# Kernel optimization log

Hardware: AMD Instinct MI355X
Metric: run time of the kernel (lower is better)

The kernel has to match this reference:

```python
import jax, jax.numpy as jnp
import numpy as np

B, S, D = 64, 1452, 1024
G, K, R = 288, 4, 32
VIS = 1152  # number of vision patch tokens; tail is S - VIS = 300 text tokens
MAX_TOKENS = 300


def setup_inputs() -> dict:
    key = jax.random.key(0)
    k1, k2, k3, k4 = jax.random.split(key, 4)
    hidden_states = jax.random.normal(k1, (B, S, D), dtype=jnp.float32)
    attention_mask = jnp.ones((B, S), dtype=jnp.int32)
    # all batches share the same vision patch range [0, VIS-1]
    patch_range_list = jnp.tile(jnp.array([[0, VIS - 1]], dtype=jnp.int32), (B, 1))
    base = jnp.broadcast_to(jnp.arange(VIS, dtype=jnp.int32).reshape(1, G, K), (B, G, K))
    drop = jax.random.uniform(k2, (B, G, K)) < 0.1
    patch_indices_list_list = jnp.where(drop, jnp.int32(-1), base)
    rem = jax.random.randint(k3, (B, R), 0, VIS, dtype=jnp.int32)
    rem = jnp.where(jax.random.uniform(k4, (B, R)) < 0.25, jnp.int32(-1), rem)
    return {
        "hidden_states": hidden_states,
        "attention_mask": attention_mask,
        "patch_range_list": patch_range_list,
        "patch_indices_list_list": patch_indices_list_list,
        "remove_index_list_list": rem,
    }


def reference(hidden_states, attention_mask, patch_range_list, patch_indices_list_list, remove_index_list_list):
    Bn, Sn, Dn = hidden_states.shape
    _, Gn, Kn = patch_indices_list_list.shape
    # vision_end_token_index is taken from batch 0 in the original and used for a
    # shape-defining slice; treat as static (identical across batches here).
    vis_end = int(patch_range_list[0, 1]) + 1

    start = patch_range_list[:, 0]            # [B]
    end = patch_range_list[:, 1]              # [B]
    L = end - start + 1                       # [B] length of sliced hidden_state

    idx = patch_indices_list_list             # [B,G,K]
    mask = idx != -1                          # [B,G,K]
    # remove_index_list: drop -1 padding (map to -2 sentinel so it never matches)
    rem = jnp.where(remove_index_list_list == -1, jnp.int32(-2), remove_index_list_list)  # [B,R]
    in_rem = (idx[..., None] == rem[:, None, None, :]).any(-1)  # torch.isin, [B,G,K]
    mask = mask & ~in_rem

    # torch gather with -1 wraps to the last element of the SLICED hidden_state;
    # replicate exactly (note: the original sums wrapped/removed entries too).
    idx_w = jnp.where(idx >= 0, idx, idx + L[:, None, None])
    gidx = start[:, None, None] + idx_w       # absolute indices into hidden_states
    gathered = jnp.take_along_axis(
        hidden_states, gidx.reshape(Bn, Gn * Kn, 1), axis=1
    ).reshape(Bn, Gn, Kn, Dn)

    cnt = mask.sum(-1)                        # [B,G] divisor = count of kept entries
    pooled = gathered.sum(2) / jnp.maximum(cnt, 1)[..., None].astype(hidden_states.dtype)

    # rows with no valid entries are dropped; survivors are written right-aligned
    valid = mask.any(-1)                      # [B,G]
    n_valid = valid.sum(1)                    # [B]
    rank = jnp.cumsum(valid, axis=1) - 1      # 0-based rank among valid rows
    pos = jnp.where(valid, MAX_TOKENS - n_valid[:, None] + rank, MAX_TOKENS)  # OOB -> drop
    bidx = jnp.arange(Bn)[:, None]

    out_head = jnp.zeros((Bn, MAX_TOKENS, Dn), hidden_states.dtype).at[bidx, pos].set(pooled, mode="drop")
    att_head = jnp.zeros((Bn, MAX_TOKENS), attention_mask.dtype).at[bidx, pos].set(1, mode="drop")

    outputs = jnp.concatenate([out_head, hidden_states[:, vis_end:]], axis=1)
    outputs_attention = jnp.concatenate([att_head, attention_mask[:, vis_end:]], axis=1)
    return outputs, outputs_attention
```

## Files before the change

### kernel.cpp

```cpp
#include <hip/hip_runtime.h>
#include <hip/hip_bf16.h>

#define Bn 64
#define Sn 1452
#define Dn 1024
#define Gn 288
#define Kn 4
#define Rn 32
#define MAXT 300

typedef float f32x4 __attribute__((ext_vector_type(4)));

__global__ void __launch_bounds__(256)
fused2_kernel(const float* __restrict__ hs,
              const int* __restrict__ idx,
              const int* __restrict__ pr,
              const int* __restrict__ rem,
              const int* __restrict__ attn,
              float* __restrict__ out,
              float* __restrict__ att_out,
              int vis_end, int T, int nheadblk, int tail4, int tailrows) {
    const int x = blockIdx.x;
    const int b = blockIdx.y;
    const int tid = threadIdx.x;

    if (x >= nheadblk) {
        const int c = x - nheadblk;
        if (tid < 4) {
            int tr = c * 4 + tid;
            if (tr < tailrows)
                att_out[(size_t)b * T + MAXT + tr] = (float)attn[b * Sn + vis_end + tr];
        }
        const f32x4* src = (const f32x4*)(hs + ((size_t)b * Sn + vis_end) * Dn);
        f32x4* dst = (f32x4*)(out + ((size_t)b * T + MAXT) * Dn);
        const int base = c * 1024;
        f32x4 v0, v1, v2, v3;
        int e0 = base + 0 * 256 + tid;
        int e1 = base + 1 * 256 + tid;
        int e2 = base + 2 * 256 + tid;
        int e3 = base + 3 * 256 + tid;
        bool p0 = e0 < tail4, p1 = e1 < tail4, p2 = e2 < tail4, p3 = e3 < tail4;
        if (p0) v0 = __builtin_nontemporal_load(&src[e0]);
        if (p1) v1 = __builtin_nontemporal_load(&src[e1]);
        if (p2) v2 = __builtin_nontemporal_load(&src[e2]);
        if (p3) v3 = __builtin_nontemporal_load(&src[e3]);
        if (p0) __builtin_nontemporal_store(v0, &dst[e0]);
        if (p1) __builtin_nontemporal_store(v1, &dst[e1]);
        if (p2) __builtin_nontemporal_store(v2, &dst[e2]);
        if (p3) __builtin_nontemporal_store(v3, &dst[e3]);
        return;
    }

    __shared__ int s_rem[Rn];
    __shared__ unsigned long long s_mask[5];
    __shared__ int s_wsum[5];
    __shared__ short s_gor[Gn];
    __shared__ char s_cnt[Gn];

    const int lane = tid & 63;
    const int w = tid >> 6;

    if (tid < Rn) {
        int r = rem[b * Rn + tid];
        s_rem[tid] = (r == -1) ? -2 : r;
    }
    __syncthreads();

    int cnt1 = 0;
    {
        const int g = tid;
#pragma unroll
        for (int k = 0; k < Kn; ++k) {
            int v = idx[(b * Gn + g) * Kn + k];
            bool m = (v != -1);
#pragma unroll
            for (int r = 0; r < Rn; ++r) m = m && (v != s_rem[r]);
            cnt1 += m ? 1 : 0;
        }
        s_cnt[g] = (char)cnt1;
    }
    int cnt2 = 0;
    if (tid < Gn - 256) {
        const int g = 256 + tid;
#pragma unroll
        for (int k = 0; k < Kn; ++k) {
            int v = idx[(b * Gn + g) * Kn + k];
            bool m = (v != -1);
#pragma unroll
            for (int r = 0; r < Rn; ++r) m = m && (v != s_rem[r]);
            cnt2 += m ? 1 : 0;
        }
        s_cnt[g] = (char)cnt2;
    }

    unsigned long long m1 = __ballot(cnt1 > 0);
    if (lane == 0) { s_mask[w] = m1; s_wsum[w] = __popcll(m1); }
    if (w == 0) {
        unsigned long long m2 = __ballot(tid < Gn - 256 && cnt2 > 0);
        if (lane == 0) { s_mask[4] = m2; s_wsum[4] = __popcll(m2); }
    }
    __syncthreads();

    int pre[5], acc = 0;
#pragma unroll
    for (int i = 0; i < 5; ++i) { pre[i] = acc; acc += s_wsum[i]; }
    const int nvalid = acc;
    const int zcut = MAXT - nvalid;

    if (cnt1 > 0) {
        int rank = pre[w] + __popcll(s_mask[w] & ((1ull << lane) - 1ull));
        s_gor[rank] = (short)tid;
    }
    if (tid < Gn - 256 && cnt2 > 0) {
        int rank = pre[4] + __popcll(s_mask[4] & ((1ull << lane) - 1ull));
        s_gor[rank] = (short)(256 + tid);
    }
    __syncthreads();

    if (tid < 2) {
        int t = 2 * x + tid;
        att_out[(size_t)b * T + t] = (t >= zcut) ? 1.0f : 0.0f;
    }

    const int start = pr[b * 2];
    const int L = pr[b * 2 + 1] - start + 1;

#pragma unroll
    for (int i = 0; i < 2; ++i) {
        const int t = 2 * x + i;
        f32x4* outp = (f32x4*)(out + ((size_t)b * T + t) * Dn);
        if (t < zcut) {
            f32x4 z = {0.f, 0.f, 0.f, 0.f};
            __builtin_nontemporal_store(z, &outp[tid]);
            continue;
        }
        const int g = s_gor[t - zcut];
        f32x4 a = {0.f, 0.f, 0.f, 0.f};
#pragma unroll
        for (int k = 0; k < Kn; ++k) {
            int v = idx[(b * Gn + g) * Kn + k];
            int wi = (v >= 0) ? v : v + L;
            const f32x4* row = (const f32x4*)(hs + ((size_t)b * Sn + start + wi) * Dn);
            a += row[tid];
        }
        const int c = (int)s_cnt[g];
        const float scale = 1.0f / (float)((c > 1) ? c : 1);
        a *= scale;
        __builtin_nontemporal_store(a, &outp[tid]);
    }
}

extern "C" void kernel_launch(void* const* d_in, const int* in_sizes, int n_in,
                              void* d_out, int out_size, void* d_ws, size_t ws_size,
                              hipStream_t stream) {
    const float* hs  = (const float*)d_in[0];
    const int* attn  = (const int*)d_in[1];
    const int* pr    = (const int*)d_in[2];
    const int* idx   = (const int*)d_in[3];
    const int* rem   = (const int*)d_in[4];

    float* out = (float*)d_out;

    const int T = out_size / (Bn * (Dn + 1));
    const int vis_end = Sn - (T - MAXT);

    float* att_out = out + (size_t)Bn * T * Dn;

    const int tailrows = T - MAXT;
    const int tail4 = tailrows * (Dn / 4);
    const int ntail = (tailrows + 3) / 4;
    const int nheadblk = (MAXT + 1) / 2;

    fused2_kernel<<<dim3(nheadblk + ntail, Bn), 256, 0, stream>>>(
        hs, idx, pr, rem, attn, out, att_out, vis_end, T, nheadblk, tail4, tailrows);
}
```

Measured before the change: 79.54 us.

## Use shared bitmap for removal lookup and double work per block

Result: slower. 103.6 us (+30.2%).

```diff
diff --git a/kernel.cpp b/kernel.cpp
--- a/kernel.cpp
+++ b/kernel.cpp
@@ -8,11 +8,12 @@
 #define Kn 4
 #define Rn 32
 #define MAXT 300
+#define BMW 18
 
 typedef float f32x4 __attribute__((ext_vector_type(4)));
 
 __global__ void __launch_bounds__(256)
-fused2_kernel(const float* __restrict__ hs,
+fused3_kernel(const float* __restrict__ hs,
               const int* __restrict__ idx,
               const int* __restrict__ pr,
               const int* __restrict__ rem,
@@ -26,32 +27,30 @@
 
     if (x >= nheadblk) {
         const int c = x - nheadblk;
-        if (tid < 4) {
-            int tr = c * 4 + tid;
+        if (tid < 8) {
+            int tr = c * 8 + tid;
             if (tr < tailrows)
                 att_out[(size_t)b * T + MAXT + tr] = (float)attn[b * Sn + vis_end + tr];
         }
         const f32x4* src = (const f32x4*)(hs + ((size_t)b * Sn + vis_end) * Dn);
         f32x4* dst = (f32x4*)(out + ((size_t)b * T + MAXT) * Dn);
-        const int base = c * 1024;
-        f32x4 v0, v1, v2, v3;
-        int e0 = base + 0 * 256 + tid;
-        int e1 = base + 1 * 256 + tid;
-        int e2 = base + 2 * 256 + tid;
-        int e3 = base + 3 * 256 + tid;
-        bool p0 = e0 < tail4, p1 = e1 < tail4, p2 = e2 < tail4, p3 = e3 < tail4;
-        if (p0) v0 = __builtin_nontemporal_load(&src[e0]);
-        if (p1) v1 = __builtin_nontemporal_load(&src[e1]);
-        if (p2) v2 = __builtin_nontemporal_load(&src[e2]);
-        if (p3) v3 = __builtin_nontemporal_load(&src[e3]);
-        if (p0) __builtin_nontemporal_store(v0, &dst[e0]);
-        if (p1) __builtin_nontemporal_store(v1, &dst[e1]);
-        if (p2) __builtin_nontemporal_store(v2, &dst[e2]);
-        if (p3) __builtin_nontemporal_store(v3, &dst[e3]);
+        const int base = c * 2048;
+        f32x4 v[8];
+        int  e[8];
+        bool p[8];
+#pragma unroll
+        for (int j = 0; j < 8; ++j) {
+            e[j] = base + j * 256 + tid;
+            p[j] = e[j] < tail4;
+            if (p[j]) v[j] = __builtin_nontemporal_load(&src[e[j]]);
+        }
+#pragma unroll
+        for (int j = 0; j < 8; ++j)
+            if (p[j]) __builtin_nontemporal_store(v[j], &dst[e[j]]);
         return;
     }
 
-    __shared__ int s_rem[Rn];
+    __shared__ unsigned long long s_bm[BMW];
     __shared__ unsigned long long s_mask[5];
     __shared__ int s_wsum[5];
     __shared__ short s_gor[Gn];
@@ -60,37 +59,42 @@
     const int lane = tid & 63;
     const int w = tid >> 6;
 
+    if (tid < BMW) s_bm[tid] = 0ull;
+    __syncthreads();
     if (tid < Rn) {
         int r = rem[b * Rn + tid];
-        s_rem[tid] = (r == -1) ? -2 : r;
+        if (r >= 0)
+            atomicOr(&s_bm[r >> 6], 1ull << (r & 63));
     }
     __syncthreads();
 
     int cnt1 = 0;
     {
-        const int g = tid;
+        const int4 gi = ((const int4*)idx)[b * Gn + tid];
+        const int vv[4] = {gi.x, gi.y, gi.z, gi.w};
 #pragma unroll
         for (int k = 0; k < Kn; ++k) {
-            int v = idx[(b * Gn + g) * Kn + k];
-            bool m = (v != -1);
-#pragma unroll
-            for (int r = 0; r < Rn; ++r) m = m && (v != s_rem[r]);
-            cnt1 += m ? 1 : 0;
+            int v = vv[k];
+            bool m = (v >= 0);
+            int word = m ? (v >> 6) : 0;
+            unsigned long long bit = (s_bm[word] >> (v & 63)) & 1ull;
+            cnt1 += (m && !bit) ? 1 : 0;
         }
-        s_cnt[g] = (char)cnt1;
+        s_cnt[tid] = (char)cnt1;
     }
     int cnt2 = 0;
     if (tid < Gn - 256) {
-        const int g = 256 + tid;
+        const int4 gi = ((const int4*)idx)[b * Gn + 256 + tid];
+        const int vv[4] = {gi.x, gi.y, gi.z, gi.w};
 #pragma unroll
         for (int k = 0; k < Kn; ++k) {
-            int v = idx[(b * Gn + g) * Kn + k];
-            bool m = (v != -1);
-#pragma unroll
-            for (int r = 0; r < Rn; ++r) m = m && (v != s_rem[r]);
-            cnt2 += m ? 1 : 0;
+            int v = vv[k];
+            bool m = (v >= 0);
+            int word = m ? (v >> 6) : 0;
+            unsigned long long bit = (s_bm[word] >> (v & 63)) & 1ull;
+            cnt2 += (m && !bit) ? 1 : 0;
         }
-        s_cnt[g] = (char)cnt2;
+        s_cnt[256 + tid] = (char)cnt2;
     }
 
     unsigned long long m1 = __ballot(cnt1 > 0);
@@ -117,8 +121,8 @@
     }
     __syncthreads();
 
-    if (tid < 2) {
-        int t = 2 * x + tid;
+    if (tid < 4) {
+        int t = 4 * x + tid;
         att_out[(size_t)b * T + t] = (t >= zcut) ? 1.0f : 0.0f;
     }
 
@@ -126,8 +130,8 @@
     const int L = pr[b * 2 + 1] - start + 1;
 
 #pragma unroll
-    for (int i = 0; i < 2; ++i) {
-        const int t = 2 * x + i;
+    for (int i = 0; i < 4; ++i) {
+        const int t = 4 * x + i;
         f32x4* outp = (f32x4*)(out + ((size_t)b * T + t) * Dn);
         if (t < zcut) {
             f32x4 z = {0.f, 0.f, 0.f, 0.f};
@@ -135,10 +139,12 @@
             continue;
         }
         const int g = s_gor[t - zcut];
+        const int4 gi = ((const int4*)idx)[b * Gn + g];
+        const int vv[4] = {gi.x, gi.y, gi.z, gi.w};
         f32x4 a = {0.f, 0.f, 0.f, 0.f};
 #pragma unroll
         for (int k = 0; k < Kn; ++k) {
-            int v = idx[(b * Gn + g) * Kn + k];
+            int v = vv[k];
             int wi = (v >= 0) ? v : v + L;
             const f32x4* row = (const f32x4*)(hs + ((size_t)b * Sn + start + wi) * Dn);
             a += row[tid];
@@ -168,9 +174,9 @@
 
     const int tailrows = T - MAXT;
     const int tail4 = tailrows * (Dn / 4);
-    const int ntail = (tailrows + 3) / 4;
-    const int nheadblk = (MAXT + 1) / 2;
+    const int ntail = (tailrows + 7) / 8;
+    const int nheadblk = (MAXT + 3) / 4;
 
-    fused2_kernel<<<dim3(nheadblk + ntail, Bn), 256, 0, stream>>>(
+    fused3_kernel<<<dim3(nheadblk + ntail, Bn), 256, 0, stream>>>(
         hs, idx, pr, rem, attn, out, att_out, vis_end, T, nheadblk, tail4, tailrows);
 }
```
